# Performance work log

Measured on AMD Instinct MI355X. Metric: run time of the kernel, lower is better.

Reference implementation:

```python
import jax, jax.numpy as jnp
import numpy as np

B, T, NA, NV, K, SD, H, E = 128, 64, 10, 16, 4, 512, 256, 32

def _lin(key, fan_in, fan_out):
    k1, k2 = jax.random.split(key)
    s = 1.0 / np.sqrt(fan_in)
    W = jax.random.uniform(k1, (fan_in, fan_out), jnp.float32, -s, s)
    b = jax.random.uniform(k2, (fan_out,), jnp.float32, -s, s)
    return W, b

def setup_inputs() -> dict:
    key = jax.random.key(0)
    ks = jax.random.split(key, 16)
    inp = {
        "qvals": jax.random.normal(ks[0], (B, T, NA), jnp.float32),
        "causal_relations": jax.random.randint(ks[1], (B, T, K, NV), 0, NA, jnp.int32),
        "states": jax.random.normal(ks[2], (B, T, SD), jnp.float32),
    }
    inp["w00_l1_W"], inp["w00_l1_b"] = _lin(ks[3], SD + NV, H)
    inp["w00_l2_W"], inp["w00_l2_b"] = _lin(ks[4], H, K)
    inp["b00_W"], inp["b00_b"] = _lin(ks[5], SD + NV, 1)
    inp["w01_W"], inp["w01_b"] = _lin(ks[6], SD, NA)
    inp["b01_W"], inp["b01_b"] = _lin(ks[7], SD, 1)
    inp["w1_l1_W"], inp["w1_l1_b"] = _lin(ks[8], SD, H)
    inp["w1_l2_W"], inp["w1_l2_b"] = _lin(ks[9], H, (NV + 1) * E)
    inp["b1_W"], inp["b1_b"] = _lin(ks[10], SD, E)
    inp["w2_l1_W"], inp["w2_l1_b"] = _lin(ks[11], SD, H)
    inp["w2_l2_W"], inp["w2_l2_b"] = _lin(ks[12], H, E)
    inp["b2_l1_W"], inp["b2_l1_b"] = _lin(ks[13], SD, E)
    inp["b2_l2_W"], inp["b2_l2_b"] = _lin(ks[14], E, 1)
    return inp

def reference(qvals, causal_relations, states,
              w00_l1_W, w00_l1_b, w00_l2_W, w00_l2_b, b00_W, b00_b,
              w01_W, w01_b, b01_W, b01_b,
              w1_l1_W, w1_l1_b, w1_l2_W, w1_l2_b, b1_W, b1_b,
              w2_l1_W, w2_l1_b, w2_l2_W, w2_l2_b,
              b2_l1_W, b2_l1_b, b2_l2_W, b2_l2_b):
    b, t, na = qvals.shape
    nv = causal_relations.shape[-1]
    sd = states.shape[-1]
    emb = b1_W.shape[1]

    # (b,t,k,nv) -> (b,t,nv,k); gather per-variable selected agent q-values
    cr = jnp.swapaxes(causal_relations, 2, 3)
    gathered = jnp.take_along_axis(qvals[:, :, None, :], cr, axis=-1)  # (b,t,nv,k)

    # Per-variable hypernets. Original builds a one-hot over n_variables but sets
    # var_onehot[variable] = 1, i.e. batch row `variable` becomes all-ones
    # (replicated faithfully). Split the first Linear into state part + onehot part:
    h_base = states @ w00_l1_W[:sd] + w00_l1_b   # (b,t,H)
    h_delta = w00_l1_W[sd:].sum(0)               # (H,)  contribution of all-ones onehot row
    g_base = states @ b00_W[:sd] + b00_b         # (b,t,1)
    g_delta = b00_W[sd:].sum(0)                  # (1,)

    def per_var(v):
        h = jax.nn.relu(h_base.at[v].add(h_delta))
        w0 = h @ w00_l2_W + w00_l2_b             # (b,t,k)
        b0 = g_base.at[v].add(g_delta)[..., 0]   # (b,t)
        return w0, b0

    w00, b00v = jax.vmap(per_var)(jnp.arange(nv))  # (nv,b,t,k), (nv,b,t)

    # group_qval_v = gathered_v @ |w0_v| + b0_v
    group = jnp.einsum('btvk,vbtk->btv', gathered, jnp.abs(w00)) + jnp.moveaxis(b00v, 0, -1)

    # residual agent mix (hyper_w0_1 / hyper_b0_1): plain linear hypernet, no abs in source
    w01 = states @ w01_W + w01_b                 # (b,t,na)
    other = jnp.einsum('bta,bta->bt', qvals, w01) + (states @ b01_W + b01_b)[..., 0]
    gq = jnp.concatenate([group, other[..., None]], axis=-1)  # (b,t,nv+1)

    # QMIX-style two-layer mix with hypernet weights
    w1 = jnp.abs((jax.nn.relu(states @ w1_l1_W + w1_l1_b) @ w1_l2_W + w1_l2_b)
                 .reshape(b, t, nv + 1, emb))
    b1 = states @ b1_W + b1_b                    # (b,t,E)
    hidden = jax.nn.elu(jnp.einsum('btv,btve->bte', gq, w1) + b1)
    w2 = jnp.abs(jax.nn.relu(states @ w2_l1_W + w2_l1_b) @ w2_l2_W + w2_l2_b)  # (b,t,E)
    b2 = jax.nn.relu(states @ b2_l1_W + b2_l1_b) @ b2_l2_W + b2_l2_b           # (b,t,1)
    y = jnp.sum(hidden * w2, axis=-1, keepdims=True) + b2
    return y  # (b,t,1)
```

## Files before the change

kernel.cpp:

```cpp
#include <hip/hip_runtime.h>
#include <hip/hip_bf16.h>


typedef __hip_bfloat16 bf16;
typedef unsigned short ushort_t;
typedef __attribute__((ext_vector_type(8))) short short8;
typedef __attribute__((ext_vector_type(4))) float f32x4;

#define PA_OFF 0
#define PA_TILES 56
#define PB_OFF (PA_TILES * 16 * 64 * 8 * 2)
#define PB_TILES 38
#define FB_OFF (PB_OFF + PB_TILES * 8 * 64 * 8 * 2)
#define NCST 2854
#define WS_NEED (size_t)(FB_OFF + NCST * 4 + 32)

#define MFMA16(a, b, c) __builtin_amdgcn_mfma_f32_16x16x32_bf16(a, b, c, 0, 0, 0)

__device__ __forceinline__ float us2f(ushort_t x) {
  unsigned u = ((unsigned)x) << 16; float f; __builtin_memcpy(&f, &u, 4); return f;
}
__device__ __forceinline__ ushort_t f2us(float v) {
  bf16 h = __float2bfloat16(v); ushort_t r; __builtin_memcpy(&r, &h, 2); return r;
}
template <bool F32>
__device__ __forceinline__ float LD(const void* p, size_t i) {
  if (F32) return ((const float*)p)[i];
  return us2f(((const ushort_t*)p)[i]);
}

__device__ __forceinline__ int detect_f32(const void* states) {
  const unsigned short* u = (const unsigned short*)states;
  int lane = threadIdx.x & 63;
  int bad = 0;
  for (int i = lane; i < 512; i += 64) {
    unsigned short x = u[i];
    int e = (x >> 7) & 0xFF;
    if (e > 140 || (((x & 0x7FFFu) != 0) && e < 100)) bad++;
  }
  for (int off = 32; off; off >>= 1) bad += __shfl_down(bad, off);
  return __shfl(bad, 0) > 20;
}

__device__ __forceinline__ void pa_store(ushort_t* pa, int np, int k, ushort_t v) {
  int t = np >> 4, lm = np & 15, ks = k >> 5, qq = (k >> 3) & 3, j = k & 7;
  pa[(size_t)t * 8192 + ks * 512 + (qq * 16 + lm) * 8 + j] = v;
}
__device__ __forceinline__ void pb_store(ushort_t* pb, int np, int k, ushort_t v) {
  int t = np >> 4, lm = np & 15, ks = k >> 5, qq = (k >> 3) & 3, j = k & 7;
  pb[(size_t)t * 4096 + ks * 512 + (qq * 16 + lm) * 8 + j] = v;
}

template <bool F32>
__device__ void prep_body(int gtid, int T, char* ws,
    const void* w00l1W, const void* w00l1b, const void* w00l2W, const void* w00l2b,
    const void* b00W, const void* b00b,
    const void* w01W, const void* w01b, const void* b01W, const void* b01b,
    const void* w1l1W, const void* w1l1b, const void* w1l2W, const void* w1l2b,
    const void* b1W, const void* b1b,
    const void* w2l1W, const void* w2l1b, const void* w2l2W, const void* w2l2b,
    const void* b2l1W, const void* b2l1b, const void* b2l2W, const void* b2l2b) {
  ushort_t* pa = (ushort_t*)(ws + PA_OFF);
  ushort_t* pb = (ushort_t*)(ws + PB_OFF);
  float* cst = (float*)(ws + FB_OFF);
  for (int i = gtid; i < 131072; i += T) {
    int k = i >> 8, n = i & 255;
    pa_store(pa, n, k, f2us(LD<F32>(w1l1W, i)));
    pa_store(pa, 256 + n, k, f2us(LD<F32>(w2l1W, i)));
    pa_store(pa, 512 + n, k, f2us(LD<F32>(w00l1W, i)));
  }
  for (int i = gtid; i < 16384; i += T) {
    int k = i >> 5, n = i & 31;
    pa_store(pa, 768 + n, k, f2us(LD<F32>(b1W, i)));
    pa_store(pa, 800 + n, k, f2us(LD<F32>(b2l1W, i)));
  }
  for (int i = gtid; i < 5120; i += T) {
    int k = i / 10, n = i % 10;
    pa_store(pa, 832 + n, k, f2us(LD<F32>(w01W, i)));
  }
  for (int i = gtid; i < 512; i += T) {
    pa_store(pa, 842, i, f2us(LD<F32>(b00W, i)));
    pa_store(pa, 843, i, f2us(LD<F32>(b01W, i)));
  }
  for (int z = gtid; z < 2048; z += T) {
    int ks = z >> 7, qq = (z >> 5) & 3, lm = 12 + ((z >> 3) & 3), j = z & 7;
    pa[(size_t)52 * 8192 + ks * 512 + (qq * 16 + lm) * 8 + j] = 0;
  }
  for (int i = gtid; i < 139264; i += T) {
    int k = i / 544, n = i % 544;
    pb_store(pb, n, k, f2us(LD<F32>(w1l2W, i)));
  }
  for (int i = gtid; i < 8192; i += T) {
    int k = i >> 5, n = i & 31;
    pb_store(pb, 544 + n, k, f2us(LD<F32>(w2l2W, i)));
  }
  for (int i = gtid; i < 8192; i += T) {
    int k = i & 255, lm = (i >> 8) & 15, tt = 36 + (i >> 12);
    ushort_t v = (lm < 4) ? f2us(LD<F32>(w00l2W, k * 4 + lm)) : (ushort_t)0;
    pb_store(pb, tt * 16 + lm, k, v);
  }
  for (int i = gtid; i < NCST; i += T) {
    float x;
    if (i < 896) {
      int c = i;
      if (c < 256) x = LD<F32>(w1l1b, c);
      else if (c < 512) x = LD<F32>(w2l1b, c - 256);
      else if (c < 768) x = LD<F32>(w00l1b, c - 512);
      else if (c < 800) x = LD<F32>(b1b, c - 768);
      else if (c < 832) x = LD<F32>(b2l1b, c - 800);
      else if (c < 842) x = LD<F32>(w01b, c - 832);
      else if (c == 842) x = LD<F32>(b00b, 0);
      else if (c == 843) x = LD<F32>(b01b, 0);
      else x = 0.f;
    } else if (i < 1536) {
      int c = i - 896;
      x = (c < 544) ? LD<F32>(w1l2b, c) : (c < 576 ? LD<F32>(w2l2b, c - 544) : 0.f);
    } else if (i < 1792) {
      int j = i - 1536; float s = 0.f;
      for (int z = 0; z < 16; ++z) s += LD<F32>(w00l1W, (size_t)(512 + z) * 256 + j);
      x = s;
    } else if (i < 2816) x = LD<F32>(w00l2W, i - 1792);
    else if (i < 2820) x = LD<F32>(w00l2b, i - 2816);
    else if (i < 2852) x = LD<F32>(b2l2W, i - 2820);
    else if (i == 2852) x = LD<F32>(b2l2b, 0);
    else { float s = 0.f; for (int z = 0; z < 16; ++z) s += LD<F32>(b00W, 512 + z); x = s; }
    cst[i] = x;
  }
}

__global__ __launch_bounds__(256) void prep_kernel(char* ws, const void* states,
    const void* w00l1W, const void* w00l1b, const void* w00l2W, const void* w00l2b,
    const void* b00W, const void* b00b,
    const void* w01W, const void* w01b, const void* b01W, const void* b01b,
    const void* w1l1W, const void* w1l1b, const void* w1l2W, const void* w1l2b,
    const void* b1W, const void* b1b,
    const void* w2l1W, const void* w2l1b, const void* w2l2W, const void* w2l2b,
    const void* b2l1W, const void* b2l1b, const void* b2l2W, const void* b2l2b) {
  int gtid = blockIdx.x * 256 + threadIdx.x;
  int T = gridDim.x * 256;
  if (detect_f32(states))
    prep_body<true>(gtid, T, ws, w00l1W, w00l1b, w00l2W, w00l2b, b00W, b00b,
        w01W, w01b, b01W, b01b, w1l1W, w1l1b, w1l2W, w1l2b, b1W, b1b,
        w2l1W, w2l1b, w2l2W, w2l2b, b2l1W, b2l1b, b2l2W, b2l2b);
  else
    prep_body<false>(gtid, T, ws, w00l1W, w00l1b, w00l2W, w00l2b, b00W, b00b,
        w01W, w01b, b01W, b01b, w1l1W, w1l1b, w1l2W, w1l2b, b1W, b1b,
        w2l1W, w2l1b, w2l2W, w2l2b, b2l1W, b2l1b, b2l2W, b2l2b);
}

struct SmemM {
  union {
    __align__(16) ushort_t sA[2][8192];
    __align__(16) ushort_t w1a[32][544];
  } u;
  __align__(16) ushort_t Am1[2][4096];
  __align__(16) ushort_t Am2[2][4096];
  __align__(16) ushort_t hbC[2][4096];
  __align__(16) ushort_t hbS[2][4096];
  float hd[256];
  float b1v[32][32];
  float rbv[32][32];
  float w2v[32][32];
  float w01v[32][12];
  float qv[32][10];
  unsigned char cr[32][64];
  float w0c[32][4], w0s[32][4];
  float gq[32][18];
  float gbv[32], b01v[32];
  float hid[32][33];
};

template <bool F32>
__device__ void mixer_body(SmemM& sm, const char* ws, int n0,
    const void* qvals, const int* crel, const void* states, void* out) {
  const int tid = threadIdx.x;
  const int lane = tid & 63, wv = tid >> 6;
  const int q = lane >> 4, lm = lane & 15;
  const int b_blk = n0 >> 6;
  const ushort_t* pa = (const ushort_t*)(ws + PA_OFF);
  const ushort_t* pb = (const ushort_t*)(ws + PB_OFF);
  const float* cstg = (const float*)(ws + FB_OFF);

  int sidx[7]; bool sreal[7];
#pragma unroll
  for (int i = 0; i < 7; ++i) {
    int s = wv + 8 * i;
    sreal[i] = (s < 53);
    sidx[i] = sreal[i] ? s : wv;
  }
  const ushort_t* baseA = pa + lane * 8;

  short8 bA[3][7];
  if (F32) {
    f32x4 va[8];
#pragma unroll
    for (int it = 0; it < 4; ++it) {
      int fi = tid + it * 512;
      int ln = fi & 63, ks = (fi >> 6) & 15, G = fi >> 10;
      int row = G * 16 + (ln & 15), col = ks * 32 + (ln >> 4) * 8;
      const f32x4* p = (const f32x4*)((const float*)states + (size_t)(n0 + row) * 512 + col);
      va[2 * it] = p[0];
      va[2 * it + 1] = p[1];
    }
#pragma unroll
    for (int d = 0; d < 3; ++d)
#pragma unroll
      for (int i = 0; i < 7; ++i)
        bA[d][i] = *(const short8*)(baseA + (size_t)sidx[i] * 8192 + d * 512);
#pragma unroll
    for (int it = 0; it < 4; ++it) {
      int fi = tid + it * 512;
      int ln = fi & 63, ks = (fi >> 6) & 15, G = fi >> 10;
      f32x4 v0 = va[2 * it], v1 = va[2 * it + 1];
      ushort_t v[8];
      v[0] = f2us(v0[0]); v[1] = f2us(v0[1]); v[2] = f2us(v0[2]); v[3] = f2us(v0[3]);
      v[4] = f2us(v1[0]); v[5] = f2us(v1[1]); v[6] = f2us(v1[2]); v[7] = f2us(v1[3]);
      *(short8*)&sm.u.sA[G][(size_t)(ks * 64 + ln) * 8] = *(short8*)v;
    }
  } else {
    short8 vb[2];
#pragma unroll
    for (int it = 0; it < 2; ++it) {
      int fi = tid + it * 512;
      int ln = fi & 63, ks = (fi >> 6) & 15, G = fi >> 10;
      int row = G * 16 + (ln & 15), col = ks * 32 + (ln >> 4) * 8;
      vb[it] = *(const short8*)((const ushort_t*)states + (size_t)(n0 + row) * 512 + col);
    }
#pragma unroll
    for (int d = 0; d < 3; ++d)
#pragma unroll
      for (int i = 0; i < 7; ++i)
        bA[d][i] = *(const short8*)(baseA + (size_t)sidx[i] * 8192 + d * 512);
#pragma unroll
    for (int it = 0; it < 2; ++it) {
      int fi = tid + it * 512;
      int ln = fi & 63, ks = (fi >> 6) & 15, G = fi >> 10;
      *(short8*)&sm.u.sA[G][(size_t)(ks * 64 + ln) * 8] = vb[it];
    }
  }
  for (int i = tid; i < 320; i += 512) sm.qv[i / 10][i % 10] = LD<F32>(qvals, (size_t)(n0 + i / 10) * 10 + i % 10);
  for (int i = tid; i < 2048; i += 512) sm.cr[i >> 6][i & 63] = (unsigned char)crel[(size_t)n0 * 64 + i];
  if (tid < 256) sm.hd[tid] = cstg[1536 + tid];
  __syncthreads();

  {
    f32x4 accA[7][2];
#pragma unroll
    for (int i = 0; i < 7; ++i) { accA[i][0] = (f32x4){0,0,0,0}; accA[i][1] = (f32x4){0,0,0,0}; }
#pragma unroll
    for (int ks = 0; ks < 16; ++ks) {
      const int d = ks % 3;
      short8 a0 = *(const short8*)&sm.u.sA[0][(ks * 64 + lane) * 8];
      short8 a1 = *(const short8*)&sm.u.sA[1][(ks * 64 + lane) * 8];
#pragma unroll
      for (int i = 0; i < 7; ++i) {
        accA[i][0] = MFMA16(a0, bA[d][i], accA[i][0]);
        accA[i][1] = MFMA16(a1, bA[d][i], accA[i][1]);
      }
      if (ks + 3 < 16) {
#pragma unroll
        for (int i = 0; i < 7; ++i)
          bA[d][i] = *(const short8*)(baseA + (size_t)sidx[i] * 8192 + (ks + 3) * 512);
      }
    }
#pragma unroll
    for (int i = 0; i < 7; ++i) {
      if (!sreal[i]) continue;
      int c = sidx[i] * 16 + lm;
      if (c >= 844) continue;
      float bias = cstg[c];
      int ks2 = (c & 255) >> 5, q2 = (c >> 3) & 3, j2 = c & 7;
      int li = (ks2 * 64 + q2 * 16 + q * 4) * 8 + j2;
#pragma unroll
      for (int G = 0; G < 2; ++G) {
        f32x4 acc = accA[i][G];
        int rb = G * 16 + q * 4;
        if (c < 256) {
#pragma unroll
          for (int g = 0; g < 4; ++g) {
            float v = acc[g] + bias;
            sm.Am1[G][li + g * 8] = f2us(v > 0.f ? v : 0.f);
          }
        } else if (c < 512) {
#pragma unroll
          for (int g = 0; g < 4; ++g) {
            float v = acc[g] + bias;
            sm.Am2[G][li + g * 8] = f2us(v > 0.f ? v : 0.f);
          }
        } else if (c < 768) {
          float hdv = sm.hd[c - 512];
#pragma unroll
          for (int g = 0; g < 4; ++g) {
            float v = acc[g] + bias;
            sm.hbC[G][li + g * 8] = f2us(v > 0.f ? v : 0.f);
            float vs = v + hdv;
            sm.hbS[G][li + g * 8] = f2us(vs > 0.f ? vs : 0.f);
          }
        } else if (c < 800) {
#pragma unroll
          for (int g = 0; g < 4; ++g) sm.b1v[rb + g][c - 768] = acc[g] + bias;
        } else if (c < 832) {
#pragma unroll
          for (int g = 0; g < 4; ++g) { float v = acc[g] + bias; sm.rbv[rb + g][c - 800] = v > 0.f ? v : 0.f; }
        } else if (c < 842) {
#pragma unroll
          for (int g = 0; g < 4; ++g) sm.w01v[rb + g][c - 832] = acc[g] + bias;
        } else if (c == 842) {
#pragma unroll
          for (int g = 0; g < 4; ++g) sm.gbv[rb + g] = acc[g] + bias;
        } else {
#pragma unroll
          for (int g = 0; g < 4; ++g) sm.b01v[rb + g] = acc[g] + bias;
        }
      }
    }
  }

  int tix[5]; bool treal[5];
#pragma unroll
  for (int i = 0; i < 5; ++i) {
    int t = wv + 8 * i;
    treal[i] = (t < 38);
    tix[i] = treal[i] ? t : wv;
  }
  const ushort_t* baseB = pb + lane * 8;
  short8 bB[3][5];
#pragma unroll
  for (int d = 0; d < 3; ++d)
#pragma unroll
    for (int i = 0; i < 5; ++i)
      bB[d][i] = *(const short8*)(baseB + (size_t)tix[i] * 4096 + d * 512);
  __syncthreads();

  {
    const ushort_t* As0[5]; const ushort_t* As1[5];
#pragma unroll
    for (int i = 0; i < 5; ++i) {
      int t = tix[i];
      As0[i] = (t < 34) ? sm.Am1[0] : (t < 36 ? sm.Am2[0] : (t == 36 ? sm.hbC[0] : sm.hbS[0]));
      As1[i] = (t < 34) ? sm.Am1[1] : (t < 36 ? sm.Am2[1] : (t == 36 ? sm.hbC[1] : sm.hbS[1]));
    }
    f32x4 accB[5][2];
#pragma unroll
    for (int i = 0; i < 5; ++i) { accB[i][0] = (f32x4){0,0,0,0}; accB[i][1] = (f32x4){0,0,0,0}; }
#pragma unroll
    for (int ks = 0; ks < 8; ++ks) {
      const int d = ks % 3;
      int ao = (ks * 64 + lane) * 8;
#pragma unroll
      for (int i = 0; i < 5; ++i) {
        short8 x0 = *(const short8*)(As0[i] + ao);
        short8 x1 = *(const short8*)(As1[i] + ao);
        accB[i][0] = MFMA16(x0, bB[d][i], accB[i][0]);
        accB[i][1] = MFMA16(x1, bB[d][i], accB[i][1]);
      }
      if (ks + 3 < 8) {
#pragma unroll
        for (int i = 0; i < 5; ++i)
          bB[d][i] = *(const short8*)(baseB + (size_t)tix[i] * 4096 + (ks + 3) * 512);
      }
    }
#pragma unroll
    for (int i = 0; i < 5; ++i) {
      if (!treal[i]) continue;
      int t = tix[i];
      int c = t * 16 + lm;
#pragma unroll
      for (int G = 0; G < 2; ++G) {
        f32x4 acc = accB[i][G];
        int rb = G * 16 + q * 4;
        if (t < 34) {
          float bias = cstg[896 + c];
#pragma unroll
          for (int g = 0; g < 4; ++g) sm.u.w1a[rb + g][c] = f2us(fabsf(acc[g] + bias));
        } else if (t < 36) {
          float bias = cstg[896 + c];
          int e = c - 544;
#pragma unroll
          for (int g = 0; g < 4; ++g) sm.w2v[rb + g][e] = fabsf(acc[g] + bias);
        } else if (t == 36) {
          if (lm < 4) {
            float bias = cstg[2816 + lm];
#pragma unroll
            for (int g = 0; g < 4; ++g) sm.w0c[rb + g][lm] = acc[g] + bias;
          }
        } else {
          if (lm < 4) {
            float bias = cstg[2816 + lm];
#pragma unroll
            for (int g = 0; g < 4; ++g) sm.w0s[rb + g][lm] = acc[g] + bias;
          }
        }
      }
    }
  }
  __syncthreads();

  {
    int r = tid >> 4, v = tid & 15;
    bool sp = (v == b_blk);
    const float* w0 = sp ? sm.w0s[r] : sm.w0c[r];
    float g = sm.gbv[r] + (sp ? cstg[2853] : 0.f);
#pragma unroll
    for (int k = 0; k < 4; ++k) {
      int a = sm.cr[r][k * 16 + v];
      g = fmaf(sm.qv[r][a], fabsf(w0[k]), g);
    }
    sm.gq[r][v] = g;
  }
  if (tid < 32) {
    float o = sm.b01v[tid];
#pragma unroll
    for (int a = 0; a < 10; ++a) o = fmaf(sm.qv[tid][a], sm.w01v[tid][a], o);
    sm.gq[tid][16] = o;
  }
  __syncthreads();

  for (int p = tid; p < 1024; p += 512) {
    int r = p >> 5, e = p & 31;
    float h = sm.b1v[r][e];
#pragma unroll
    for (int v = 0; v < 17; ++v) h = fmaf(sm.gq[r][v], us2f(sm.u.w1a[r][v * 32 + e]), h);
    float hid = h > 0.f ? h : (expf(h) - 1.f);
    sm.hid[r][e] = hid * sm.w2v[r][e] + sm.rbv[r][e] * cstg[2820 + e];
  }
  __syncthreads();

  if (tid < 32) {
    float y = cstg[2852];
#pragma unroll
    for (int e = 0; e < 32; ++e) y += sm.hid[tid][e];
    if (F32) ((float*)out)[n0 + tid] = y;
    else ((bf16*)out)[n0 + tid] = __float2bfloat16(y);
  }
}

__global__ __launch_bounds__(512, 2) void causal_mixer_mfma(const char* ws,
    const void* qvals, const int* crel, const void* states, void* out) {
  __shared__ SmemM sm;
  int n0 = blockIdx.x * 32;
  if (detect_f32(states))
    mixer_body<true>(sm, ws, n0, qvals, crel, states, out);
  else
    mixer_body<false>(sm, ws, n0, qvals, crel, states, out);
}

extern "C" void kernel_launch(void* const* d_in, const int* in_sizes, int n_in,
                              void* d_out, int out_size, void* d_ws, size_t ws_size,
                              hipStream_t stream) {
  char* ws = (char*)d_ws;
  hipLaunchKernelGGL(prep_kernel, dim3(512), dim3(256), 0, stream, ws, d_in[2],
      d_in[3], d_in[4], d_in[5], d_in[6], d_in[7], d_in[8],
      d_in[9], d_in[10], d_in[11], d_in[12],
      d_in[13], d_in[14], d_in[15], d_in[16], d_in[17], d_in[18],
      d_in[19], d_in[20], d_in[21], d_in[22], d_in[23], d_in[24],
      d_in[25], d_in[26]);
  hipLaunchKernelGGL(causal_mixer_mfma, dim3(256), dim3(512), 0, stream, ws,
      d_in[0], (const int*)d_in[1], d_in[2], d_out);
}
```

Baseline: 147.7 us.

## Double mixer block to 1024 threads, spreading MFMA tiles over 16 waves

The mixer kernel now launches 1024 threads per block (16 waves) instead of 512, so each wave handles at most 4 stage-A and 3 stage-B MFMA column tiles instead of 7 and 5. Padding tiles are zero-filled and skip their global B-fragment loads, where before they issued redundant loads. The elementwise stages are remapped so each thread handles one item. The aim is more latency hiding and less serial MFMA work per wave, at the cost of launch_bounds(1024,4) squeezing registers per thread, which may cause spills, and more idle waves in the small epilogue stages.

```diff
diff --git a/kernel.cpp b/kernel.cpp
--- a/kernel.cpp
+++ b/kernel.cpp
@@ -180,22 +180,23 @@
   const ushort_t* pa = (const ushort_t*)(ws + PA_OFF);
   const ushort_t* pb = (const ushort_t*)(ws + PB_OFF);
   const float* cstg = (const float*)(ws + FB_OFF);
-
-  int sidx[7]; bool sreal[7];
-#pragma unroll
-  for (int i = 0; i < 7; ++i) {
-    int s = wv + 8 * i;
+  const short8 z8 = {0, 0, 0, 0, 0, 0, 0, 0};
+
+  int sidx[4]; bool sreal[4];
+#pragma unroll
+  for (int i = 0; i < 4; ++i) {
+    int s = wv + 16 * i;
     sreal[i] = (s < 53);
-    sidx[i] = sreal[i] ? s : wv;
+    sidx[i] = sreal[i] ? s : 0;
   }
   const ushort_t* baseA = pa + lane * 8;
 
-  short8 bA[3][7];
+  short8 bA[3][4];
   if (F32) {
-    f32x4 va[8];
-#pragma unroll
-    for (int it = 0; it < 4; ++it) {
-      int fi = tid + it * 512;
+    f32x4 va[4];
+#pragma unroll
+    for (int it = 0; it < 2; ++it) {
+      int fi = tid + it * 1024;
       int ln = fi & 63, ks = (fi >> 6) & 15, G = fi >> 10;
       int row = G * 16 + (ln & 15), col = ks * 32 + (ln >> 4) * 8;
       const f32x4* p = (const f32x4*)((const float*)states + (size_t)(n0 + row) * 512 + col);
@@ -203,13 +204,19 @@
       va[2 * it + 1] = p[1];
     }
 #pragma unroll
-    for (int d = 0; d < 3; ++d)
-#pragma unroll
-      for (int i = 0; i < 7; ++i)
-        bA[d][i] = *(const short8*)(baseA + (size_t)sidx[i] * 8192 + d * 512);
-#pragma unroll
-    for (int it = 0; it < 4; ++it) {
-      int fi = tid + it * 512;
+    for (int i = 0; i < 4; ++i) {
+      if (sreal[i]) {
+#pragma unroll
+        for (int d = 0; d < 3; ++d)
+          bA[d][i] = *(const short8*)(baseA + (size_t)sidx[i] * 8192 + d * 512);
+      } else {
+#pragma unroll
+        for (int d = 0; d < 3; ++d) bA[d][i] = z8;
+      }
+    }
+#pragma unroll
+    for (int it = 0; it < 2; ++it) {
+      int fi = tid + it * 1024;
       int ln = fi & 63, ks = (fi >> 6) & 15, G = fi >> 10;
       f32x4 v0 = va[2 * it], v1 = va[2 * it + 1];
       ushort_t v[8];
@@ -221,50 +228,57 @@
     short8 vb[2];
 #pragma unroll
     for (int it = 0; it < 2; ++it) {
-      int fi = tid + it * 512;
+      int fi = tid + it * 1024;
       int ln = fi & 63, ks = (fi >> 6) & 15, G = fi >> 10;
       int row = G * 16 + (ln & 15), col = ks * 32 + (ln >> 4) * 8;
       vb[it] = *(const short8*)((const ushort_t*)states + (size_t)(n0 + row) * 512 + col);
     }
 #pragma unroll
-    for (int d = 0; d < 3; ++d)
-#pragma unroll
-      for (int i = 0; i < 7; ++i)
-        bA[d][i] = *(const short8*)(baseA + (size_t)sidx[i] * 8192 + d * 512);
+    for (int i = 0; i < 4; ++i) {
+      if (sreal[i]) {
+#pragma unroll
+        for (int d = 0; d < 3; ++d)
+          bA[d][i] = *(const short8*)(baseA + (size_t)sidx[i] * 8192 + d * 512);
+      } else {
+#pragma unroll
+        for (int d = 0; d < 3; ++d) bA[d][i] = z8;
+      }
+    }
 #pragma unroll
     for (int it = 0; it < 2; ++it) {
-      int fi = tid + it * 512;
+      int fi = tid + it * 1024;
       int ln = fi & 63, ks = (fi >> 6) & 15, G = fi >> 10;
       *(short8*)&sm.u.sA[G][(size_t)(ks * 64 + ln) * 8] = vb[it];
     }
   }
-  for (int i = tid; i < 320; i += 512) sm.qv[i / 10][i % 10] = LD<F32>(qvals, (size_t)(n0 + i / 10) * 10 + i % 10);
-  for (int i = tid; i < 2048; i += 512) sm.cr[i >> 6][i & 63] = (unsigned char)crel[(size_t)n0 * 64 + i];
+  for (int i = tid; i < 320; i += 1024) sm.qv[i / 10][i % 10] = LD<F32>(qvals, (size_t)(n0 + i / 10) * 10 + i % 10);
+  for (int i = tid; i < 2048; i += 1024) sm.cr[i >> 6][i & 63] = (unsigned char)crel[(size_t)n0 * 64 + i];
   if (tid < 256) sm.hd[tid] = cstg[1536 + tid];
   __syncthreads();
 
   {
-    f32x4 accA[7][2];
-#pragma unroll
-    for (int i = 0; i < 7; ++i) { accA[i][0] = (f32x4){0,0,0,0}; accA[i][1] = (f32x4){0,0,0,0}; }
+    f32x4 accA[4][2];
+#pragma unroll
+    for (int i = 0; i < 4; ++i) { accA[i][0] = (f32x4){0,0,0,0}; accA[i][1] = (f32x4){0,0,0,0}; }
 #pragma unroll
     for (int ks = 0; ks < 16; ++ks) {
       const int d = ks % 3;
       short8 a0 = *(const short8*)&sm.u.sA[0][(ks * 64 + lane) * 8];
       short8 a1 = *(const short8*)&sm.u.sA[1][(ks * 64 + lane) * 8];
 #pragma unroll
-      for (int i = 0; i < 7; ++i) {
+      for (int i = 0; i < 4; ++i) {
         accA[i][0] = MFMA16(a0, bA[d][i], accA[i][0]);
         accA[i][1] = MFMA16(a1, bA[d][i], accA[i][1]);
       }
       if (ks + 3 < 16) {
 #pragma unroll
-        for (int i = 0; i < 7; ++i)
-          bA[d][i] = *(const short8*)(baseA + (size_t)sidx[i] * 8192 + (ks + 3) * 512);
-      }
-    }
-#pragma unroll
-    for (int i = 0; i < 7; ++i) {
+        for (int i = 0; i < 4; ++i)
+          if (sreal[i])
+            bA[d][i] = *(const short8*)(baseA + (size_t)sidx[i] * 8192 + (ks + 3) * 512);
+      }
+    }
+#pragma unroll
+    for (int i = 0; i < 4; ++i) {
       if (!sreal[i]) continue;
       int c = sidx[i] * 16 + lm;
       if (c >= 844) continue;
@@ -316,39 +330,45 @@
     }
   }
 
-  int tix[5]; bool treal[5];
-#pragma unroll
-  for (int i = 0; i < 5; ++i) {
-    int t = wv + 8 * i;
+  int tix[3]; bool treal[3];
+#pragma unroll
+  for (int i = 0; i < 3; ++i) {
+    int t = wv + 16 * i;
     treal[i] = (t < 38);
-    tix[i] = treal[i] ? t : wv;
+    tix[i] = treal[i] ? t : 0;
   }
   const ushort_t* baseB = pb + lane * 8;
-  short8 bB[3][5];
-#pragma unroll
-  for (int d = 0; d < 3; ++d)
-#pragma unroll
-    for (int i = 0; i < 5; ++i)
-      bB[d][i] = *(const short8*)(baseB + (size_t)tix[i] * 4096 + d * 512);
+  short8 bB[3][3];
+#pragma unroll
+  for (int i = 0; i < 3; ++i) {
+    if (treal[i]) {
+#pragma unroll
+      for (int d = 0; d < 3; ++d)
+        bB[d][i] = *(const short8*)(baseB + (size_t)tix[i] * 4096 + d * 512);
+    } else {
+#pragma unroll
+      for (int d = 0; d < 3; ++d) bB[d][i] = z8;
+    }
+  }
   __syncthreads();
 
   {
-    const ushort_t* As0[5]; const ushort_t* As1[5];
-#pragma unroll
-    for (int i = 0; i < 5; ++i) {
+    const ushort_t* As0[3]; const ushort_t* As1[3];
+#pragma unroll
+    for (int i = 0; i < 3; ++i) {
       int t = tix[i];
       As0[i] = (t < 34) ? sm.Am1[0] : (t < 36 ? sm.Am2[0] : (t == 36 ? sm.hbC[0] : sm.hbS[0]));
       As1[i] = (t < 34) ? sm.Am1[1] : (t < 36 ? sm.Am2[1] : (t == 36 ? sm.hbC[1] : sm.hbS[1]));
     }
-    f32x4 accB[5][2];
-#pragma unroll
-    for (int i = 0; i < 5; ++i) { accB[i][0] = (f32x4){0,0,0,0}; accB[i][1] = (f32x4){0,0,0,0}; }
+    f32x4 accB[3][2];
+#pragma unroll
+    for (int i = 0; i < 3; ++i) { accB[i][0] = (f32x4){0,0,0,0}; accB[i][1] = (f32x4){0,0,0,0}; }
 #pragma unroll
     for (int ks = 0; ks < 8; ++ks) {
       const int d = ks % 3;
       int ao = (ks * 64 + lane) * 8;
 #pragma unroll
-      for (int i = 0; i < 5; ++i) {
+      for (int i = 0; i < 3; ++i) {
         short8 x0 = *(const short8*)(As0[i] + ao);
         short8 x1 = *(const short8*)(As1[i] + ao);
         accB[i][0] = MFMA16(x0, bB[d][i], accB[i][0]);
@@ -356,12 +376,13 @@
       }
       if (ks + 3 < 8) {
 #pragma unroll
-        for (int i = 0; i < 5; ++i)
-          bB[d][i] = *(const short8*)(baseB + (size_t)tix[i] * 4096 + (ks + 3) * 512);
-      }
-    }
-#pragma unroll
-    for (int i = 0; i < 5; ++i) {
+        for (int i = 0; i < 3; ++i)
+          if (treal[i])
+            bB[d][i] = *(const short8*)(baseB + (size_t)tix[i] * 4096 + (ks + 3) * 512);
+      }
+    }
+#pragma unroll
+    for (int i = 0; i < 3; ++i) {
       if (!treal[i]) continue;
       int t = tix[i];
       int c = t * 16 + lm;
@@ -396,7 +417,7 @@
   }
   __syncthreads();
 
-  {
+  if (tid < 512) {
     int r = tid >> 4, v = tid & 15;
     bool sp = (v == b_blk);
     const float* w0 = sp ? sm.w0s[r] : sm.w0c[r];
@@ -416,8 +437,8 @@
   }
   __syncthreads();
 
-  for (int p = tid; p < 1024; p += 512) {
-    int r = p >> 5, e = p & 31;
+  {
+    int r = tid >> 5, e = tid & 31;
     float h = sm.b1v[r][e];
 #pragma unroll
     for (int v = 0; v < 17; ++v) h = fmaf(sm.gq[r][v], us2f(sm.u.w1a[r][v * 32 + e]), h);
@@ -435,7 +456,7 @@
   }
 }
 
-__global__ __launch_bounds__(512, 2) void causal_mixer_mfma(const char* ws,
+__global__ __launch_bounds__(1024, 4) void causal_mixer_mfma(const char* ws,
     const void* qvals, const int* crel, const void* states, void* out) {
   __shared__ SmemM sm;
   int n0 = blockIdx.x * 32;
@@ -455,6 +476,6 @@
       d_in[13], d_in[14], d_in[15], d_in[16], d_in[17], d_in[18],
       d_in[19], d_in[20], d_in[21], d_in[22], d_in[23], d_in[24],
       d_in[25], d_in[26]);
-  hipLaunchKernelGGL(causal_mixer_mfma, dim3(256), dim3(512), 0, stream, ws,
+  hipLaunchKernelGGL(causal_mixer_mfma, dim3(256), dim3(1024), 0, stream, ws,
       d_in[0], (const int*)d_in[1], d_in[2], d_out);
 }
```

New measurement: 140.3 us. -5.0%, faster.
